# Kernel tuning notes

Hardware: AMD Instinct MI355X
Metric: run time of the kernel (lower is better)

The kernel has to match this reference:

```python
import jax, jax.numpy as jnp
import numpy as np

HIDDEN = 4096
NQ = 32        # query heads
NKV = 8        # kv heads
HD = 128       # head dim
EPS = 1e-6
BASE = 10000.0
T = 2048


def setup_inputs() -> dict:
    key = jax.random.key(0)
    ks = jax.random.split(key, 4)
    s = 0.02
    return {
        "hidden_states": jax.random.normal(ks[0], (T, HIDDEN), jnp.float32),
        "w_qkv": jax.random.normal(ks[1], ((NQ + 2 * NKV) * HD, HIDDEN), jnp.float32) * s,
        "q_norm_w": jnp.ones((HD,), jnp.float32),
        "k_norm_w": jnp.ones((HD,), jnp.float32),
        "w_o": jax.random.normal(ks[2], (HIDDEN, NQ * HD), jnp.float32) * s,
        "positions": jnp.arange(T, dtype=jnp.int64),
    }


def _rms_norm(x, w):
    # x: [T, H, D], normalize over last dim
    var = jnp.mean(jnp.square(x), axis=-1, keepdims=True)
    return x * jax.lax.rsqrt(var + EPS) * w


def _rope(x, positions):
    # neox-style: split halves. x: [T, H, D]
    half = HD // 2
    inv_freq = 1.0 / (BASE ** (jnp.arange(0, HD, 2, dtype=jnp.float32) / HD))  # [half]
    ang = positions.astype(jnp.float32)[:, None] * inv_freq  # [T, half]
    cos = jnp.cos(ang)[:, None, :]  # [T, 1, half]
    sin = jnp.sin(ang)[:, None, :]
    x1, x2 = x[..., :half], x[..., half:]
    return jnp.concatenate([x1 * cos - x2 * sin, x2 * cos + x1 * sin], axis=-1)


def reference(hidden_states, w_qkv, q_norm_w, k_norm_w, w_o, positions):
    t = hidden_states.shape[0]
    qkv = hidden_states @ w_qkv.T  # [T, (NQ+2*NKV)*HD]
    q, k, v = jnp.split(qkv, [NQ * HD, (NQ + NKV) * HD], axis=-1)
    q = _rms_norm(q.reshape(t, NQ, HD), q_norm_w)
    k = _rms_norm(k.reshape(t, NKV, HD), k_norm_w)
    v = v.reshape(t, NKV, HD)
    q = _rope(q, positions)
    k = _rope(k, positions)

    g = NQ // NKV
    qg = q.reshape(t, NKV, g, HD).transpose(1, 2, 0, 3)  # [NKV, g, T, HD]
    kt = k.transpose(1, 0, 2)  # [NKV, T, HD]
    vt = v.transpose(1, 0, 2)
    scale = HD ** -0.5
    scores = jnp.einsum('hgqd,hkd->hgqk', qg, kt) * scale  # [NKV, g, T, T]
    causal = positions[:, None] >= positions[None, :]  # [T, T]
    scores = jnp.where(causal[None, None], scores, jnp.float32(-1e30))
    p = jax.nn.softmax(scores, axis=-1)
    o = jnp.einsum('hgqk,hkd->hgqd', p, vt)  # [NKV, g, T, HD]
    o = o.transpose(2, 0, 1, 3).reshape(t, NQ * HD)
    return o @ w_o.T
```

## Files before the change

### kernel.cpp

```cpp
#include <hip/hip_runtime.h>
#include <hip/hip_bf16.h>

typedef float f32x4 __attribute__((ext_vector_type(4)));
typedef short s16x8 __attribute__((ext_vector_type(8)));
typedef short s16x4 __attribute__((ext_vector_type(4)));
typedef unsigned short u16;

#define HIDDEN 4096
#define NQ 32
#define NKV 8
#define HD 128
#define T_SEQ 2048
#define QKV_N ((NQ + 2 * NKV) * HD)

__device__ __forceinline__ u16 f2bf(float f) {
    union { float f; unsigned u; } v; v.f = f;
    unsigned r = v.u + 0x7FFFu + ((v.u >> 16) & 1u);
    return (u16)(r >> 16);
}
__device__ __forceinline__ float b2f(u16 h) {
    union { unsigned u; float f; } v; v.u = ((unsigned)h) << 16; return v.f;
}
__device__ __forceinline__ void gload_lds16(const u16* g, u16* l) {
    __builtin_amdgcn_global_load_lds(
        (const __attribute__((address_space(1))) unsigned int*)g,
        (__attribute__((address_space(3))) unsigned int*)l,
        16, 0, 0);
}
__device__ __forceinline__ int xcd_swz(int flat, int nwg) {
    return (flat & 7) * (nwg >> 3) + (flat >> 3);
}

__device__ __forceinline__ void conv8(const float* src, u16* dst, int i) {
    const float4 a = ((const float4*)src)[2 * i];
    const float4 b = ((const float4*)src)[2 * i + 1];
    s16x8 o;
    o[0] = (short)f2bf(a.x); o[1] = (short)f2bf(a.y);
    o[2] = (short)f2bf(a.z); o[3] = (short)f2bf(a.w);
    o[4] = (short)f2bf(b.x); o[5] = (short)f2bf(b.y);
    o[6] = (short)f2bf(b.z); o[7] = (short)f2bf(b.w);
    ((s16x8*)dst)[i] = o;
}
__global__ __launch_bounds__(256) void conv_bf16_kern(
    const float* __restrict__ src, u16* __restrict__ dst, int n8)
{
    for (int i = blockIdx.x * 256 + threadIdx.x; i < n8; i += gridDim.x * 256)
        conv8(src, dst, i);
}
__global__ __launch_bounds__(256) void conv2_bf16_kern(
    const float* __restrict__ s1, u16* __restrict__ d1, int n1,
    const float* __restrict__ s2, u16* __restrict__ d2, int n2)
{
    for (int i = blockIdx.x * 256 + threadIdx.x; i < n1 + n2; i += gridDim.x * 256) {
        if (i < n1) conv8(s1, d1, i);
        else        conv8(s2, d2, i - n1);
    }
}

template<int OUT_BF16>
__global__ __launch_bounds__(256) void gemm_bt_bf16(
    const u16* __restrict__ A, const u16* __restrict__ B,
    void* __restrict__ Cv, int N, int K)
{
    __shared__ u16 As[2][128 * 32];
    __shared__ u16 Bs[2][128 * 32];
    const int tid = threadIdx.x, lane = tid & 63, wid = tid >> 6;
    const int wr = wid >> 1, wc = wid & 1, lg = lane >> 4, l15 = lane & 15;
    const int m0 = blockIdx.y * 128, n0 = blockIdx.x * 128;
    const int srow = wid * 32 + (lane >> 2);
    const int scol = (((lane & 3) ^ ((lane >> 3) & 3))) * 8;
    const u16* ga = &A[(size_t)(m0 + srow) * K + scol];
    const u16* gb = &B[(size_t)(n0 + srow) * K + scol];
    const int rsw = (lg ^ ((l15 >> 1) & 3)) * 8;

    f32x4 acc[4][4] = {};
    const int nk = K >> 5;

    auto stage = [&](int buf, int koff) {
        u16* la = &As[buf][wid * 1024];
        u16* lb = &Bs[buf][wid * 1024];
        gload_lds16(ga + koff, la);
        gload_lds16(ga + koff + 16 * K, la + 512);
        gload_lds16(gb + koff, lb);
        gload_lds16(gb + koff + 16 * K, lb + 512);
    };

    stage(0, 0);
    for (int kk = 0; kk < nk; ++kk) {
        const int cur = kk & 1;
        if (kk + 1 < nk) {
            stage(cur ^ 1, (kk + 1) * 32);
            asm volatile("s_waitcnt vmcnt(4)" ::: "memory");
        } else {
            asm volatile("s_waitcnt vmcnt(0)" ::: "memory");
        }
        __builtin_amdgcn_s_barrier();
        s16x8 af[4], bfr[4];
#pragma unroll
        for (int i = 0; i < 4; ++i) af[i]  = *(const s16x8*)&As[cur][(wr * 64 + i * 16 + l15) * 32 + rsw];
#pragma unroll
        for (int j = 0; j < 4; ++j) bfr[j] = *(const s16x8*)&Bs[cur][(wc * 64 + j * 16 + l15) * 32 + rsw];
#pragma unroll
        for (int i = 0; i < 4; ++i)
#pragma unroll
            for (int j = 0; j < 4; ++j)
                acc[i][j] = __builtin_amdgcn_mfma_f32_16x16x32_bf16(af[i], bfr[j], acc[i][j], 0, 0, 0);
        __builtin_amdgcn_s_barrier();
    }
#pragma unroll
    for (int i = 0; i < 4; ++i) {
        int r0 = m0 + wr * 64 + i * 16 + lg * 4;
#pragma unroll
        for (int j = 0; j < 4; ++j) {
            int cc = n0 + wc * 64 + j * 16 + l15;
#pragma unroll
            for (int r = 0; r < 4; ++r) {
                if (OUT_BF16)
                    ((u16*)Cv)[(size_t)(r0 + r) * N + cc] = f2bf(acc[i][j][r]);
                else
                    ((float*)Cv)[(size_t)(r0 + r) * N + cc] = acc[i][j][r];
            }
        }
    }
}

__global__ __launch_bounds__(256) void norm_rope_kern(
    const u16* __restrict__ qkv, const float* __restrict__ qw,
    const float* __restrict__ kw, u16* __restrict__ qr, u16* __restrict__ kr)
{
    const int t = blockIdx.x, h = blockIdx.y * 4 + (threadIdx.x >> 6);
    const int i = threadIdx.x & 63;
    const size_t rowbase = (size_t)t * QKV_N;
    const u16* src; const float* w; u16* dst;
    if (h < 32) {
        src = qkv + rowbase + h * HD; w = qw;
        dst = qr + ((size_t)h * T_SEQ + t) * HD;
    } else {
        int kh = h - 32;
        src = qkv + rowbase + NQ * HD + kh * HD; w = kw;
        dst = kr + ((size_t)kh * T_SEQ + t) * HD;
    }
    float x1 = b2f(src[i]), x2 = b2f(src[i + 64]);
    float ss = x1 * x1 + x2 * x2;
#pragma unroll
    for (int d = 32; d >= 1; d >>= 1) ss += __shfl_xor(ss, d);
    float rs = rsqrtf(ss * (1.0f / 128.0f) + 1e-6f);
    x1 *= rs * w[i];
    x2 *= rs * w[i + 64];
    float ang = (float)t * exp2f((float)i * -0.20762050593567985f);
    float sn, cs;
    sincosf(ang, &sn, &cs);
    dst[i]      = f2bf(x1 * cs - x2 * sn);
    dst[i + 64] = f2bf(x2 * cs + x1 * sn);
}

__global__ __launch_bounds__(256) void vtrans_kern(
    const u16* __restrict__ qkv, u16* __restrict__ vt)
{
    __shared__ u16 Ts[128][66];
    const int t0 = blockIdx.x * 64, kh = blockIdx.y, tid = threadIdx.x;
#pragma unroll
    for (int it = 0; it < 4; ++it) {
        int slot = tid + it * 256;
        int tl = slot >> 4, dc = (slot & 15) * 8;
        s16x8 v = *(const s16x8*)&qkv[(size_t)(t0 + tl) * QKV_N + (NQ + NKV) * HD + kh * HD + dc];
#pragma unroll
        for (int e = 0; e < 8; ++e) Ts[dc + e][tl] = (u16)v[e];
    }
    __syncthreads();
#pragma unroll
    for (int it = 0; it < 4; ++it) {
        int slot = tid + it * 256;
        int d = slot >> 3, c = (slot & 7) * 8;
        s16x8 v = *(const s16x8*)&Ts[d][c];
        *(s16x8*)&vt[((size_t)kh * HD + d) * T_SEQ + t0 + c] = v;
    }
}

#define KS(b, r, c) Ks[(b)][((r) << 7) + ((c) ^ (((r) & 7) << 3))]
#define VS(b, r, c) Vs[(b)][((r) << 6) + ((c) ^ (((r) & 7) << 3))]
#define PS(wv, r, c) Ps[((wv) << 10) + ((r) << 6) + ((c) ^ (((r) & 7) << 3))]

__global__ __launch_bounds__(512) void attn_kern(
    const u16* __restrict__ qr, const u16* __restrict__ kr,
    const u16* __restrict__ vt, u16* __restrict__ o)
{
    __shared__ u16 Ks[2][64 * 128];
    __shared__ u16 Vs[2][128 * 64];
    __shared__ u16 Ps[8 * 16 * 64];
    const int tid = threadIdx.x, lane = tid & 63, w = tid >> 6;
    const int lg = lane >> 4, l15 = lane & 15;
    const int flat = xcd_swz((int)blockIdx.y * 8 + (int)blockIdx.x, 256);
    const int qh = flat >> 3, bx = flat & 7;
    const int kvh = qh >> 2;
    const float scale2 = 0.08838834764831845f * 1.4426950408889634f;

    const int krow = tid >> 4, kcol = (tid & 15) * 8;
    const int vrow = tid >> 3, vcol = (tid & 7) * 8;
    const u16* krbase = kr + (size_t)kvh * T_SEQ * HD;
    const u16* vtbase = vt + (size_t)kvh * HD * T_SEQ;

    s16x8 kst[2], vst[2];
#define LOADKV(k0_) do { \
    kst[0] = *(const s16x8*)&krbase[(size_t)((k0_) + krow) * HD + kcol]; \
    kst[1] = *(const s16x8*)&krbase[(size_t)((k0_) + krow + 32) * HD + kcol]; \
    vst[0] = *(const s16x8*)&vtbase[(size_t)(vrow) * T_SEQ + (k0_) + vcol]; \
    vst[1] = *(const s16x8*)&vtbase[(size_t)(vrow + 64) * T_SEQ + (k0_) + vcol]; \
    } while (0)
#define WRITEKV(b) do { \
    *(s16x8*)&KS((b), krow, kcol) = kst[0]; \
    *(s16x8*)&KS((b), krow + 32, kcol) = kst[1]; \
    *(s16x8*)&VS((b), vrow, vcol) = vst[0]; \
    *(s16x8*)&VS((b), vrow + 64, vcol) = vst[1]; \
    } while (0)

    for (int half = 0; half < 2; ++half) {
        const int q0 = (half == 0) ? bx * 128 : (T_SEQ - 128) - bx * 128;
        s16x8 qf[4];
        {
            const u16* qb = qr + ((size_t)qh * T_SEQ + q0 + w * 16 + l15) * HD;
#pragma unroll
            for (int dc = 0; dc < 4; ++dc) qf[dc] = *(const s16x8*)&qb[dc * 32 + lg * 8];
        }
        f32x4 oacc[8] = {};
        float mQ = -1e30f, lsQ = 0.f;

        const int ktiles = (q0 >> 6) + 2;
        LOADKV(0);
        WRITEKV(0);
        __syncthreads();
        for (int kt = 0; kt < ktiles; ++kt) {
            const int k0 = kt * 64;
            const int cur = kt & 1;
            if (kt + 1 < ktiles) LOADKV(k0 + 64);

            f32x4 sc[4] = {};
            __builtin_amdgcn_s_setprio(1);
#pragma unroll
            for (int nc = 0; nc < 4; ++nc)
#pragma unroll
                for (int dc = 0; dc < 4; ++dc) {
                    s16x8 kf = *(const s16x8*)&KS(cur, nc * 16 + l15, dc * 32 + lg * 8);
                    sc[nc] = __builtin_amdgcn_mfma_f32_16x16x32_bf16(kf, qf[dc], sc[nc], 0, 0, 0);
                }
            __builtin_amdgcn_s_setprio(0);

            const int qg = q0 + w * 16 + l15;
            const bool needMask = (k0 + 63) > (q0 + w * 16);
            float tm = -1e30f;
#pragma unroll
            for (int nc = 0; nc < 4; ++nc)
#pragma unroll
                for (int r = 0; r < 4; ++r) {
                    float v = sc[nc][r] * scale2;
                    int kg = k0 + nc * 16 + lg * 4 + r;
                    if (needMask && kg > qg) v = -1e30f;
                    sc[nc][r] = v;
                    tm = fmaxf(tm, v);
                }
            tm = fmaxf(tm, __shfl_xor(tm, 16));
            tm = fmaxf(tm, __shfl_xor(tm, 32));

            if (__any(tm > mQ + 8.0f)) {
                float mn = fmaxf(mQ, tm);
                float alpha = exp2f(mQ - mn);
                mQ = mn;
                lsQ *= alpha;
                float aq[4];
#pragma unroll
                for (int r = 0; r < 4; ++r) aq[r] = __shfl(alpha, lg * 4 + r);
#pragma unroll
                for (int dc = 0; dc < 8; ++dc)
#pragma unroll
                    for (int r = 0; r < 4; ++r) oacc[dc][r] *= aq[r];
            }

            float ts = 0.f;
#pragma unroll
            for (int nc = 0; nc < 4; ++nc) {
                s16x4 pk;
#pragma unroll
                for (int r = 0; r < 4; ++r) {
                    float e = exp2f(sc[nc][r] - mQ);
                    ts += e;
                    pk[r] = (short)f2bf(e);
                }
                *(s16x4*)&PS(w, l15, nc * 16 + lg * 4) = pk;
            }
            ts += __shfl_xor(ts, 16);
            ts += __shfl_xor(ts, 32);
            lsQ += ts;

            __builtin_amdgcn_s_setprio(1);
#pragma unroll
            for (int kc = 0; kc < 2; ++kc) {
                s16x8 pf = *(const s16x8*)&PS(w, l15, kc * 32 + lg * 8);
#pragma unroll
                for (int dc = 0; dc < 8; ++dc) {
                    s16x8 vf = *(const s16x8*)&VS(cur, dc * 16 + l15, kc * 32 + lg * 8);
                    oacc[dc] = __builtin_amdgcn_mfma_f32_16x16x32_bf16(pf, vf, oacc[dc], 0, 0, 0);
                }
            }
            __builtin_amdgcn_s_setprio(0);

            if (kt + 1 < ktiles) WRITEKV(cur ^ 1);
            __syncthreads();
        }
        float lq[4];
#pragma unroll
        for (int r = 0; r < 4; ++r) lq[r] = __shfl(lsQ, lg * 4 + r);
#pragma unroll
        for (int r = 0; r < 4; ++r) {
            float inv = 1.0f / lq[r];
            int trow = q0 + w * 16 + lg * 4 + r;
            u16* dst = o + (size_t)trow * (NQ * HD) + qh * HD;
#pragma unroll
            for (int dc = 0; dc < 8; ++dc) dst[dc * 16 + l15] = f2bf(oacc[dc][r] * inv);
        }
    }
#undef LOADKV
#undef WRITEKV
}

extern "C" void kernel_launch(void* const* d_in, const int* in_sizes, int n_in,
                              void* d_out, int out_size, void* d_ws, size_t ws_size,
                              hipStream_t stream)
{
    const float* hs   = (const float*)d_in[0];
    const float* wqkv = (const float*)d_in[1];
    const float* qw   = (const float*)d_in[2];
    const float* kw   = (const float*)d_in[3];
    const float* wo   = (const float*)d_in[4];
    float* out = (float*)d_out;

    char* ws = (char*)d_ws;
    u16* hs_bf   = (u16*)(ws);
    u16* ob      = (u16*)(ws);
    u16* wqkv_bf = (u16*)(ws + 16777216);
    u16* qr      = (u16*)(ws + 16777216);
    u16* kr      = (u16*)(ws + 33554432);
    u16* vt      = (u16*)(ws + 37748736);
    u16* wo_bf   = (u16*)(ws + 41943040);
    u16* qkv_bf  = (u16*)(ws + 67108864);

    conv2_bf16_kern<<<2048, 256, 0, stream>>>(
        hs, hs_bf, T_SEQ * HIDDEN / 8, wqkv, wqkv_bf, QKV_N * HIDDEN / 8);
    gemm_bt_bf16<1><<<dim3(QKV_N / 128, T_SEQ / 128), 256, 0, stream>>>(
        hs_bf, wqkv_bf, (void*)qkv_bf, QKV_N, HIDDEN);
    norm_rope_kern<<<dim3(T_SEQ, 10), 256, 0, stream>>>(qkv_bf, qw, kw, qr, kr);
    vtrans_kern<<<dim3(T_SEQ / 64, NKV), 256, 0, stream>>>(qkv_bf, vt);
    conv_bf16_kern<<<2048, 256, 0, stream>>>(wo, wo_bf, HIDDEN * HIDDEN / 8);
    attn_kern<<<dim3(8, NQ), 512, 0, stream>>>(qr, kr, vt, ob);
    gemm_bt_bf16<0><<<dim3(HIDDEN / 128, T_SEQ / 128), 256, 0, stream>>>(
        ob, wo_bf, (void*)out, HIDDEN, HIDDEN);
}
```

Baseline: 349.9 us.

## Merge norm-rope with V transpose and fold wo conversion into attention launch

Norm+RoPE and the V transpose are combined into one kernel whose block range is split between the two jobs. The separate wo fp32-to-bf16 conversion kernel is removed. Its work now runs on extra blocks of the attention grid (odd blockIdx.x), so it overlaps with the attention blocks. This cuts two launches and lets the memory-bound conversion share the GPU with the compute-bound attention. The risk is that conversion blocks take CU slots or bandwidth the attention blocks would otherwise use.

```diff
diff --git a/kernel.cpp b/kernel.cpp
--- a/kernel.cpp
+++ b/kernel.cpp
@@ -40,12 +40,6 @@
     o[4] = (short)f2bf(b.x); o[5] = (short)f2bf(b.y);
     o[6] = (short)f2bf(b.z); o[7] = (short)f2bf(b.w);
     ((s16x8*)dst)[i] = o;
-}
-__global__ __launch_bounds__(256) void conv_bf16_kern(
-    const float* __restrict__ src, u16* __restrict__ dst, int n8)
-{
-    for (int i = blockIdx.x * 256 + threadIdx.x; i < n8; i += gridDim.x * 256)
-        conv8(src, dst, i);
 }
 __global__ __launch_bounds__(256) void conv2_bf16_kern(
     const float* __restrict__ s1, u16* __restrict__ d1, int n1,
@@ -124,41 +118,42 @@
     }
 }
 
-__global__ __launch_bounds__(256) void norm_rope_kern(
+__global__ __launch_bounds__(256) void nr_vt_kern(
     const u16* __restrict__ qkv, const float* __restrict__ qw,
-    const float* __restrict__ kw, u16* __restrict__ qr, u16* __restrict__ kr)
-{
-    const int t = blockIdx.x, h = blockIdx.y * 4 + (threadIdx.x >> 6);
-    const int i = threadIdx.x & 63;
-    const size_t rowbase = (size_t)t * QKV_N;
-    const u16* src; const float* w; u16* dst;
-    if (h < 32) {
-        src = qkv + rowbase + h * HD; w = qw;
-        dst = qr + ((size_t)h * T_SEQ + t) * HD;
-    } else {
-        int kh = h - 32;
-        src = qkv + rowbase + NQ * HD + kh * HD; w = kw;
-        dst = kr + ((size_t)kh * T_SEQ + t) * HD;
-    }
-    float x1 = b2f(src[i]), x2 = b2f(src[i + 64]);
-    float ss = x1 * x1 + x2 * x2;
-#pragma unroll
-    for (int d = 32; d >= 1; d >>= 1) ss += __shfl_xor(ss, d);
-    float rs = rsqrtf(ss * (1.0f / 128.0f) + 1e-6f);
-    x1 *= rs * w[i];
-    x2 *= rs * w[i + 64];
-    float ang = (float)t * exp2f((float)i * -0.20762050593567985f);
-    float sn, cs;
-    sincosf(ang, &sn, &cs);
-    dst[i]      = f2bf(x1 * cs - x2 * sn);
-    dst[i + 64] = f2bf(x2 * cs + x1 * sn);
-}
-
-__global__ __launch_bounds__(256) void vtrans_kern(
-    const u16* __restrict__ qkv, u16* __restrict__ vt)
+    const float* __restrict__ kw, u16* __restrict__ qr, u16* __restrict__ kr,
+    u16* __restrict__ vt)
 {
     __shared__ u16 Ts[128][66];
-    const int t0 = blockIdx.x * 64, kh = blockIdx.y, tid = threadIdx.x;
+    const int id = blockIdx.x, tid = threadIdx.x;
+    if (id < 20480) {
+        const int t = id & 2047, h = (id >> 11) * 4 + (tid >> 6);
+        const int i = tid & 63;
+        const size_t rowbase = (size_t)t * QKV_N;
+        const u16* src; const float* w; u16* dst;
+        if (h < 32) {
+            src = qkv + rowbase + h * HD; w = qw;
+            dst = qr + ((size_t)h * T_SEQ + t) * HD;
+        } else {
+            int kh = h - 32;
+            src = qkv + rowbase + NQ * HD + kh * HD; w = kw;
+            dst = kr + ((size_t)kh * T_SEQ + t) * HD;
+        }
+        float x1 = b2f(src[i]), x2 = b2f(src[i + 64]);
+        float ss = x1 * x1 + x2 * x2;
+#pragma unroll
+        for (int d = 32; d >= 1; d >>= 1) ss += __shfl_xor(ss, d);
+        float rs = rsqrtf(ss * (1.0f / 128.0f) + 1e-6f);
+        x1 *= rs * w[i];
+        x2 *= rs * w[i + 64];
+        float ang = (float)t * exp2f((float)i * -0.20762050593567985f);
+        float sn, cs;
+        sincosf(ang, &sn, &cs);
+        dst[i]      = f2bf(x1 * cs - x2 * sn);
+        dst[i + 64] = f2bf(x2 * cs + x1 * sn);
+        return;
+    }
+    const int id2 = id - 20480;
+    const int t0 = (id2 & 31) * 64, kh = id2 >> 5;
 #pragma unroll
     for (int it = 0; it < 4; ++it) {
         int slot = tid + it * 256;
@@ -183,14 +178,23 @@
 
 __global__ __launch_bounds__(512) void attn_kern(
     const u16* __restrict__ qr, const u16* __restrict__ kr,
-    const u16* __restrict__ vt, u16* __restrict__ o)
+    const u16* __restrict__ vt, u16* __restrict__ o,
+    const float* __restrict__ wo, u16* __restrict__ wo_bf)
 {
     __shared__ u16 Ks[2][64 * 128];
     __shared__ u16 Vs[2][128 * 64];
     __shared__ u16 Ps[8 * 16 * 64];
-    const int tid = threadIdx.x, lane = tid & 63, w = tid >> 6;
+    const int tid = threadIdx.x;
+    if (blockIdx.x & 1) {
+        const int task = (int)blockIdx.y * 8 + ((int)blockIdx.x >> 1);
+        const int base = task * 8192 + tid;
+#pragma unroll
+        for (int it = 0; it < 16; ++it) conv8(wo, wo_bf, base + it * 512);
+        return;
+    }
+    const int lane = tid & 63, w = tid >> 6;
     const int lg = lane >> 4, l15 = lane & 15;
-    const int flat = xcd_swz((int)blockIdx.y * 8 + (int)blockIdx.x, 256);
+    const int flat = xcd_swz((int)blockIdx.y * 8 + ((int)blockIdx.x >> 1), 256);
     const int qh = flat >> 3, bx = flat & 7;
     const int kvh = qh >> 2;
     const float scale2 = 0.08838834764831845f * 1.4426950408889634f;
@@ -347,10 +351,8 @@
         hs, hs_bf, T_SEQ * HIDDEN / 8, wqkv, wqkv_bf, QKV_N * HIDDEN / 8);
     gemm_bt_bf16<1><<<dim3(QKV_N / 128, T_SEQ / 128), 256, 0, stream>>>(
         hs_bf, wqkv_bf, (void*)qkv_bf, QKV_N, HIDDEN);
-    norm_rope_kern<<<dim3(T_SEQ, 10), 256, 0, stream>>>(qkv_bf, qw, kw, qr, kr);
-    vtrans_kern<<<dim3(T_SEQ / 64, NKV), 256, 0, stream>>>(qkv_bf, vt);
-    conv_bf16_kern<<<2048, 256, 0, stream>>>(wo, wo_bf, HIDDEN * HIDDEN / 8);
-    attn_kern<<<dim3(8, NQ), 512, 0, stream>>>(qr, kr, vt, ob);
+    nr_vt_kern<<<20736, 256, 0, stream>>>(qkv_bf, qw, kw, qr, kr, vt);
+    attn_kern<<<dim3(16, NQ), 512, 0, stream>>>(qr, kr, vt, ob, wo, wo_bf);
     gemm_bt_bf16<0><<<dim3(HIDDEN / 128, T_SEQ / 128), 256, 0, stream>>>(
         ob, wo_bf, (void*)out, HIDDEN, HIDDEN);
 }
```

After: 399.8 us. +14.2%, slower.
